# Performance work log

Hardware: AMD Instinct MI355X
Metric: run time of the kernel (lower is better)

## Reference

```python
import jax, jax.numpy as jnp
import numpy as np

B, T, D, H, S = 512, 256, 128, 128, 32


def _param(key, shape, scale):
    return (jax.random.normal(key, shape, dtype=jnp.float32) * scale)


def setup_inputs() -> dict:
    key = jax.random.key(0)
    ks = jax.random.split(key, 32)
    sD = 1.0 / np.sqrt(D)
    sH = 1.0 / np.sqrt(H)
    inp = {
        'x': jax.random.normal(ks[0], (B, T, D), dtype=jnp.float32),
        'statics': jax.random.normal(ks[1], (B, S), dtype=jnp.float32),
        'mask': (jax.random.uniform(ks[2], (B, T, D)) > 0.5).astype(jnp.float32),
        'delta': jax.random.uniform(ks[3], (B, T, D), dtype=jnp.float32),
        'x_last_observed': jax.random.normal(ks[4], (B, T, D), dtype=jnp.float32),
        'x_mean': jax.random.normal(ks[5], (B, D), dtype=jnp.float32),
        'hs0': jax.random.normal(ks[6], (B, H), dtype=jnp.float32),
        # GRU-D decay params
        'w_dg_x': _param(ks[7], (D,), sD), 'b_dg_x': jnp.zeros((D,), jnp.float32),
        'W_dg_h': _param(ks[8], (H, D), sD), 'b_dg_h': jnp.zeros((H,), jnp.float32),
        # gates: update z, reset r, candidate h
        'W_z': _param(ks[9], (H, D), sD), 'U_z': _param(ks[10], (H, H), sH),
        'V_z': _param(ks[11], (H, D), sD), 'b_z': jnp.zeros((H,), jnp.float32),
        'W_r': _param(ks[12], (H, D), sD), 'U_r': _param(ks[13], (H, H), sH),
        'V_r': _param(ks[14], (H, D), sD), 'b_r': jnp.zeros((H,), jnp.float32),
        'W_h': _param(ks[15], (H, D), sD), 'U_h': _param(ks[16], (H, H), sH),
        'V_h': _param(ks[17], (H, D), sD), 'b_h': jnp.zeros((H,), jnp.float32),
        # classifier
        'W_out': _param(ks[18], (1, H + S), 1.0 / np.sqrt(H + S)),
        'b_out': jnp.zeros((1,), jnp.float32),
    }
    return inp


def reference(x, statics, mask, delta, x_last_observed, x_mean, hs0,
              w_dg_x, b_dg_x, W_dg_h, b_dg_h,
              W_z, U_z, V_z, b_z, W_r, U_r, V_r, b_r,
              W_h, U_h, V_h, b_h, W_out, b_out):
    # scan over time: inputs [T, B, D]
    xs = jnp.transpose(x, (1, 0, 2))
    ms = jnp.transpose(mask, (1, 0, 2))
    ds = jnp.transpose(delta, (1, 0, 2))
    xl = jnp.transpose(x_last_observed, (1, 0, 2))

    def step(h, inputs):
        xv, m, d, xlast = inputs
        gamma_x = jnp.exp(-jax.nn.relu(w_dg_x * d + b_dg_x))            # [B, D]
        gamma_h = jnp.exp(-jax.nn.relu(d @ W_dg_h.T + b_dg_h))          # [B, H]
        x_hat = m * xv + (1.0 - m) * (gamma_x * xlast + (1.0 - gamma_x) * x_mean)
        h = gamma_h * h
        z = jax.nn.sigmoid(x_hat @ W_z.T + h @ U_z.T + m @ V_z.T + b_z)
        r = jax.nn.sigmoid(x_hat @ W_r.T + h @ U_r.T + m @ V_r.T + b_r)
        h_tilde = jnp.tanh(x_hat @ W_h.T + (r * h) @ U_h.T + m @ V_h.T + b_h)
        h = (1.0 - z) * h + z * h_tilde
        return h, None

    h_final, _ = jax.lax.scan(step, hs0, (xs, ms, ds, xl))
    full = jnp.concatenate([h_final, statics], axis=1)                  # [B, H+S]
    predictions = full @ W_out.T + b_out                                # [B, 1]
    return predictions
```

## Files before the change

### kernel.cpp

```cpp
#include <hip/hip_runtime.h>
#include <stdint.h>


#define B_ 512
#define T_ 256
#define D_ 128
#define H_ 128
#define S_ 32
#define NE 512
#define KA 384
#define M_ (B_*T_)
#define HP 136
#define ESLAB ((size_t)NE * 16)
#define ESTRIDE ((size_t)32 * ESLAB)

typedef __attribute__((ext_vector_type(8))) short short8;
typedef __attribute__((ext_vector_type(4))) float f32x4;

#define BAR_LDS() asm volatile("s_waitcnt lgkmcnt(0)\n\ts_barrier" ::: "memory")

__device__ __forceinline__ unsigned short f2bf(float f) {
  union { float f; uint32_t u; } v; v.f = f;
  return (unsigned short)((v.u + 0x7FFFu + ((v.u >> 16) & 1u)) >> 16);
}
__device__ __forceinline__ unsigned short f2bf_fast(float f) {
  union { float f; uint32_t u; } v; v.f = f;
  return (unsigned short)((v.u + 0x8000u) >> 16);
}
__device__ __forceinline__ float bf2f(uint32_t s) {
  union { uint32_t u; float f; } v; v.u = s << 16;
  return v.f;
}

__device__ __forceinline__ uint2  ldraw(const unsigned short* p) { return *(const uint2*)p; }
__device__ __forceinline__ float4 ldraw(const float* p)          { return *(const float4*)p; }
__device__ __forceinline__ void unp(uint2 v, float o[4]) {
  o[0] = bf2f(v.x & 0xffffu); o[1] = bf2f(v.x >> 16);
  o[2] = bf2f(v.y & 0xffffu); o[3] = bf2f(v.y >> 16);
}
__device__ __forceinline__ void unp(float4 v, float o[4]) {
  o[0] = v.x; o[1] = v.y; o[2] = v.z; o[3] = v.w;
}
__device__ __forceinline__ void st4(unsigned short* p, const float v[4]) {
  uint2 u;
  u.x = (uint32_t)f2bf(v[0]) | ((uint32_t)f2bf(v[1]) << 16);
  u.y = (uint32_t)f2bf(v[2]) | ((uint32_t)f2bf(v[3]) << 16);
  *(uint2*)p = u;
}
__device__ __forceinline__ void st4(float* p, const float v[4]) {
  *(float4*)p = make_float4(v[0], v[1], v[2], v[3]);
}

__device__ __forceinline__ float fsigmoid(float x) {
  return __builtin_amdgcn_rcpf(1.f + __expf(-x));
}
__device__ __forceinline__ float ftanh(float x) {
  return 1.f - 2.f * __builtin_amdgcn_rcpf(1.f + __expf(2.f * x));
}

#define ASYNC_CP16(gsrc, ldst) \
  __builtin_amdgcn_global_load_lds((const __attribute__((address_space(1))) void*)(gsrc), \
                                   (__attribute__((address_space(3))) void*)(ldst), 16, 0, 0)

__global__ void prep_weights(const float* __restrict__ Wz, const float* __restrict__ Vz,
                             const float* __restrict__ Wr, const float* __restrict__ Vr,
                             const float* __restrict__ Wh, const float* __restrict__ Vh,
                             const float* __restrict__ Wdgh,
                             const float* __restrict__ bz, const float* __restrict__ br,
                             const float* __restrict__ bh, const float* __restrict__ bdgh,
                             unsigned short* __restrict__ Wcat, float* __restrict__ bias)
{
  int id = blockIdx.x * 256 + threadIdx.x;
  if (id < NE * KA) {
    int n = id / KA, k = id - n * KA;
    float v = 0.f;
    if (n < 384) {
      int nn = n & 127;
      const float* W = (n < 128) ? Wz : (n < 256) ? Wr : Wh;
      const float* V = (n < 128) ? Vz : (n < 256) ? Vr : Vh;
      if (k < 128)      v = W[nn * 128 + k];
      else if (k < 256) v = V[nn * 128 + (k - 128)];
    } else {
      if (k >= 256) v = Wdgh[(n - 384) * 128 + (k - 256)];
    }
    Wcat[id] = f2bf(v);
  }
  if (id < NE) {
    bias[id] = (id < 128) ? bz[id] : (id < 256) ? br[id - 128]
             : (id < 384) ? bh[id - 256] : bdgh[id - 384];
  }
}

__global__ void build_A(const float* __restrict__ x, const float* __restrict__ mask,
                        const float* __restrict__ delta, const float* __restrict__ xlast,
                        const float* __restrict__ xmean,
                        const float* __restrict__ wdgx, const float* __restrict__ bdgx,
                        unsigned short* __restrict__ Abuf)
{
  int id = blockIdx.x * 256 + threadIdx.x;
  int m = id >> 5;
  int c = id & 31;
  int t = m >> 9;
  int b = m & (B_ - 1);
  int k = c * 4;
  size_t src = ((size_t)b * T_ + t) * D_ + k;
  float4 xv = *(const float4*)(x + src);
  float4 mv = *(const float4*)(mask + src);
  float4 dv = *(const float4*)(delta + src);
  float4 lv = *(const float4*)(xlast + src);
  float4 uv = *(const float4*)(xmean + (size_t)b * D_ + k);
  float4 wv = *(const float4*)(wdgx + k);
  float4 bv = *(const float4*)(bdgx + k);
  const float* xp = (const float*)&xv; const float* mp = (const float*)&mv;
  const float* dp = (const float*)&dv; const float* lp = (const float*)&lv;
  const float* up = (const float*)&uv; const float* wp = (const float*)&wv;
  const float* bp = (const float*)&bv;
  unsigned short xh[4], mm[4], dd[4];
  #pragma unroll
  for (int i = 0; i < 4; ++i) {
    float g = __expf(-fmaxf(wp[i] * dp[i] + bp[i], 0.f));
    float xhat = mp[i] * xp[i] + (1.f - mp[i]) * (g * lp[i] + (1.f - g) * up[i]);
    xh[i] = f2bf(xhat); mm[i] = f2bf(mp[i]); dd[i] = f2bf(dp[i]);
  }
  uint2 px, pm, pd;
  px.x = (uint32_t)xh[0] | ((uint32_t)xh[1] << 16); px.y = (uint32_t)xh[2] | ((uint32_t)xh[3] << 16);
  pm.x = (uint32_t)mm[0] | ((uint32_t)mm[1] << 16); pm.y = (uint32_t)mm[2] | ((uint32_t)mm[3] << 16);
  pd.x = (uint32_t)dd[0] | ((uint32_t)dd[1] << 16); pd.y = (uint32_t)dd[2] | ((uint32_t)dd[3] << 16);
  unsigned short* rowp = Abuf + (size_t)m * KA;
  *(uint2*)(rowp + k)       = px;
  *(uint2*)(rowp + 128 + k) = pm;
  *(uint2*)(rowp + 256 + k) = pd;
}

template <typename ET>
__global__ __launch_bounds__(256, 2) void gemm_phase1(
    const unsigned short* __restrict__ Abuf, const unsigned short* __restrict__ Wcat,
    const float* __restrict__ bias, ET* __restrict__ E)
{
  __shared__ unsigned short As[3][4096];
  __shared__ unsigned short Bs[3][4096];
  const int tid = threadIdx.x;
  const int wave = tid >> 6, lane = tid & 63;
  const int q = lane >> 4, rl = lane & 15;
  const int m0 = blockIdx.x * 128;
  const int n0 = blockIdx.y * 128;
  const int wm = (wave >> 1) * 64, wn = (wave & 1) * 64;

  f32x4 acc[4][4];
  #pragma unroll
  for (int a = 0; a < 4; ++a)
    #pragma unroll
    for (int b = 0; b < 4; ++b) acc[a][b] = (f32x4){0.f, 0.f, 0.f, 0.f};

  #define STAGE(kt_) do {                                                     \
    const int kbase_ = (kt_) * 32; const int buf_ = (kt_) % 3;                \
    _Pragma("unroll")                                                         \
    for (int i = 0; i < 2; ++i) {                                             \
      int chunk = i * 256 + wave * 64 + lane;                                 \
      int row = chunk >> 2, kc = chunk & 3;                                   \
      ASYNC_CP16(Abuf + (size_t)(m0 + row) * KA + kbase_ + kc * 8,            \
                 &As[buf_][(i * 256 + wave * 64) * 8]);                       \
      ASYNC_CP16(Wcat + (size_t)(n0 + row) * KA + kbase_ + kc * 8,            \
                 &Bs[buf_][(i * 256 + wave * 64) * 8]);                       \
    }                                                                         \
  } while (0)

  STAGE(0);
  STAGE(1);

  #pragma unroll
  for (int kt = 0; kt < 12; ++kt) {
    if (kt == 11) asm volatile("s_waitcnt vmcnt(0)" ::: "memory");
    else          asm volatile("s_waitcnt vmcnt(4)" ::: "memory");
    asm volatile("s_barrier" ::: "memory");
    if (kt < 10) STAGE(kt + 2);
    const int buf = kt % 3;
    short8 af[4], bfr[4];
    #pragma unroll
    for (int tm = 0; tm < 4; ++tm)
      af[tm] = *(const short8*)(&As[buf][(wm + tm * 16 + rl) * 32 + q * 8]);
    #pragma unroll
    for (int tn = 0; tn < 4; ++tn)
      bfr[tn] = *(const short8*)(&Bs[buf][(wn + tn * 16 + rl) * 32 + q * 8]);
    #pragma unroll
    for (int tm = 0; tm < 4; ++tm)
      #pragma unroll
      for (int tn = 0; tn < 4; ++tn)
        acc[tm][tn] = __builtin_amdgcn_mfma_f32_16x16x32_bf16(af[tm], bfr[tn], acc[tm][tn], 0, 0, 0);
  }
  #undef STAGE

  const int t = m0 >> 9;
  const int bbase = m0 & (B_ - 1);
  #pragma unroll
  for (int tn = 0; tn < 4; ++tn) {
    int n = n0 + wn + tn * 16 + rl;
    float bv = bias[n];
    bool isg = (n >= 384);
    #pragma unroll
    for (int tm = 0; tm < 4; ++tm) {
      int brow = bbase + wm + tm * 16;
      float v[4];
      #pragma unroll
      for (int reg = 0; reg < 4; ++reg) {
        float xv = acc[tm][tn][reg] + bv;
        v[reg] = isg ? __expf(-fmaxf(xv, 0.f)) : xv;
      }
      st4(E + ((size_t)t * 32 + (brow >> 4)) * ESLAB + (size_t)n * 16 + q * 4, v);
    }
  }
}

template <typename ET>
__global__ __launch_bounds__(512, 2) void grud_scan(
    const ET* __restrict__ E,
    const float* __restrict__ Uz, const float* __restrict__ Ur, const float* __restrict__ Uh,
    const float* __restrict__ hs0, const float* __restrict__ statics,
    const float* __restrict__ Wout, const float* __restrict__ bout,
    float* __restrict__ out)
{
  __shared__ unsigned short hdec[16 * HP];
  __shared__ unsigned short rhb[16 * HP];
  __shared__ float hfin[16 * HP];
  const int tid = threadIdx.x;
  const int wave = tid >> 6, lane = tid & 63;
  const int q = lane >> 4, rl = lane & 15;
  const int col = wave * 16 + rl;
  const int b0 = blockIdx.x * 16;

  short8 uz[4], ur[4], uh[4];
  #pragma unroll
  for (int kc = 0; kc < 4; ++kc) {
    int koff = kc * 32 + q * 8;
    const float* pzw = Uz + col * H_ + koff;
    const float* prw = Ur + col * H_ + koff;
    const float* phw = Uh + col * H_ + koff;
    #pragma unroll
    for (int j = 0; j < 8; ++j) {
      uz[kc][j] = (short)f2bf(pzw[j]);
      ur[kc][j] = (short)f2bf(prw[j]);
      uh[kc][j] = (short)f2bf(phw[j]);
    }
  }

  const ET* pz = E + (size_t)blockIdx.x * ESLAB + (size_t)col * 16 + q * 4;
  const ET* pr = pz + 128 * 16;
  const ET* ph = pz + 256 * 16;
  const ET* pg = pz + 384 * 16;

  using RawT = decltype(ldraw((const ET*)nullptr));
  RawT cz, cr, chh, cg, nz{}, nr{}, nh{}, ng{};
  cz  = ldraw(pz);
  cr  = ldraw(pr);
  chh = ldraw(ph);
  cg  = ldraw(pg + ESTRIDE);
  RawT g0raw = ldraw(pg);

  float hd[4], g0[4];
  unp(g0raw, g0);
  #pragma unroll
  for (int reg = 0; reg < 4; ++reg) {
    int row = q * 4 + reg;
    float h0 = hs0[(b0 + row) * H_ + col];
    hd[reg] = g0[reg] * h0;
    hdec[row * HP + col] = f2bf_fast(hd[reg]);
  }
  BAR_LDS();

  for (int t = 0; t < T_; ++t) {
    if (t + 1 < T_) {
      size_t off = (size_t)(t + 1) * ESTRIDE;
      nz = ldraw(pz + off); nr = ldraw(pr + off); nh = ldraw(ph + off);
      if (t + 2 < T_) ng = ldraw(pg + (size_t)(t + 2) * ESTRIDE);
    }
    float Pz[4], Pr[4], Ph[4];
    unp(cz, Pz); unp(cr, Pr); unp(chh, Ph);

    short8 af[4];
    #pragma unroll
    for (int kc = 0; kc < 4; ++kc)
      af[kc] = *(const short8*)(&hdec[rl * HP + kc * 32 + q * 8]);
    f32x4 accz = (f32x4){0.f,0.f,0.f,0.f}, accr = (f32x4){0.f,0.f,0.f,0.f};
    #pragma unroll
    for (int kc = 0; kc < 4; ++kc) {
      accz = __builtin_amdgcn_mfma_f32_16x16x32_bf16(af[kc], uz[kc], accz, 0, 0, 0);
      accr = __builtin_amdgcn_mfma_f32_16x16x32_bf16(af[kc], ur[kc], accr, 0, 0, 0);
    }
    float zz[4];
    #pragma unroll
    for (int reg = 0; reg < 4; ++reg) {
      zz[reg] = fsigmoid(accz[reg] + Pz[reg]);
      float rr = fsigmoid(accr[reg] + Pr[reg]);
      rhb[(q * 4 + reg) * HP + col] = f2bf_fast(rr * hd[reg]);
    }
    BAR_LDS();

    short8 ar[4];
    #pragma unroll
    for (int kc = 0; kc < 4; ++kc)
      ar[kc] = *(const short8*)(&rhb[rl * HP + kc * 32 + q * 8]);
    f32x4 acch = (f32x4){0.f,0.f,0.f,0.f};
    #pragma unroll
    for (int kc = 0; kc < 4; ++kc)
      acch = __builtin_amdgcn_mfma_f32_16x16x32_bf16(ar[kc], uh[kc], acch, 0, 0, 0);

    if (t < T_ - 1) {
      float Gn[4];
      unp(cg, Gn);
      #pragma unroll
      for (int reg = 0; reg < 4; ++reg) {
        float ht = ftanh(acch[reg] + Ph[reg]);
        float hn = hd[reg] + zz[reg] * (ht - hd[reg]);
        hd[reg] = Gn[reg] * hn;
        hdec[(q * 4 + reg) * HP + col] = f2bf_fast(hd[reg]);
      }
    } else {
      #pragma unroll
      for (int reg = 0; reg < 4; ++reg) {
        float ht = ftanh(acch[reg] + Ph[reg]);
        float hn = hd[reg] + zz[reg] * (ht - hd[reg]);
        hfin[(q * 4 + reg) * HP + col] = hn;
      }
    }
    BAR_LDS();

    cz = nz; cr = nr; chh = nh; cg = ng;
  }

  {
    int row = tid >> 5, j = tid & 31;
    float acc = 0.f;
    #pragma unroll
    for (int c0 = 0; c0 < 4; ++c0)
      acc += hfin[row * HP + j + c0 * 32] * Wout[j + c0 * 32];
    acc += statics[(size_t)(b0 + row) * S_ + j] * Wout[H_ + j];
    #pragma unroll
    for (int off = 16; off >= 1; off >>= 1)
      acc += __shfl_down(acc, off, 32);
    if (j == 0) out[b0 + row] = acc + bout[0];
  }
}

template <typename ET>
static void launch_all(void* const* d_in, float* out, char* ws, hipStream_t stream)
{
  const float* x      = (const float*)d_in[0];
  const float* statics= (const float*)d_in[1];
  const float* mask   = (const float*)d_in[2];
  const float* delta  = (const float*)d_in[3];
  const float* xlast  = (const float*)d_in[4];
  const float* xmean  = (const float*)d_in[5];
  const float* hs0    = (const float*)d_in[6];
  const float* wdgx   = (const float*)d_in[7];
  const float* bdgx   = (const float*)d_in[8];
  const float* Wdgh   = (const float*)d_in[9];
  const float* bdgh   = (const float*)d_in[10];
  const float* Wz     = (const float*)d_in[11];
  const float* Uz     = (const float*)d_in[12];
  const float* Vz     = (const float*)d_in[13];
  const float* bz     = (const float*)d_in[14];
  const float* Wr     = (const float*)d_in[15];
  const float* Ur     = (const float*)d_in[16];
  const float* Vr     = (const float*)d_in[17];
  const float* br     = (const float*)d_in[18];
  const float* Wh     = (const float*)d_in[19];
  const float* Uh     = (const float*)d_in[20];
  const float* Vh     = (const float*)d_in[21];
  const float* bh     = (const float*)d_in[22];
  const float* Wout   = (const float*)d_in[23];
  const float* bout   = (const float*)d_in[24];

  const size_t eBytes = (size_t)M_ * NE * sizeof(ET);
  const size_t aBytes = (size_t)M_ * KA * 2;
  const size_t wBytes = (size_t)NE * KA * 2;
  ET* E = (ET*)ws;
  unsigned short* Abuf = (unsigned short*)(ws + eBytes);
  unsigned short* Wcat = (unsigned short*)(ws + eBytes + aBytes);
  float* bias = (float*)(ws + eBytes + aBytes + wBytes);

  prep_weights<<<768, 256, 0, stream>>>(Wz, Vz, Wr, Vr, Wh, Vh, Wdgh,
                                        bz, br, bh, bdgh, Wcat, bias);
  build_A<<<(M_ * 32) / 256, 256, 0, stream>>>(x, mask, delta, xlast, xmean,
                                               wdgx, bdgx, Abuf);
  gemm_phase1<ET><<<dim3(M_ / 128, NE / 128), 256, 0, stream>>>(Abuf, Wcat, bias, E);
  grud_scan<ET><<<B_ / 16, 512, 0, stream>>>(E, Uz, Ur, Uh, hs0, statics, Wout, bout, out);
}

extern "C" void kernel_launch(void* const* d_in, const int* in_sizes, int n_in,
                              void* d_out, int out_size, void* d_ws, size_t ws_size,
                              hipStream_t stream)
{
  char* ws = (char*)d_ws;
  float* out = (float*)d_out;
  const size_t common = (size_t)M_ * KA * 2 + (size_t)NE * KA * 2 + 8192;
  const size_t needF32 = (size_t)M_ * NE * 4 + common;
  const size_t needBF  = (size_t)M_ * NE * 2 + common;
  if (ws_size >= needF32)     launch_all<float>(d_in, out, ws, stream);
  else if (ws_size >= needBF) launch_all<unsigned short>(d_in, out, ws, stream);
}
```

Measured before the change: 597.5 us.

## Skip zero K-tiles for decay-gate GEMM block and halve scan waves

In the input-projection GEMM, the column block that computes the hidden-state decay gate now starts at K-tile 8. Those output columns depend only on the delta section of the concatenated input, so the x-hat and mask tiles are never loaded or multiplied there. The loop is no longer fully unrolled, which makes the triple-buffer index dynamic, and the occupancy hint is raised. The recurrent scan kernel drops from 8 waves to 4 per block, with each wave handling two 16-column groups, to make the three block barriers per timestep cheaper. It also moves the z-gate sigmoid after the first barrier so it can overlap the h-candidate MFMAs, at the cost of more registers per thread.

```diff
diff --git a/kernel.cpp b/kernel.cpp
--- a/kernel.cpp
+++ b/kernel.cpp
@@ -133,7 +133,7 @@
 }
 
 template <typename ET>
-__global__ __launch_bounds__(256, 2) void gemm_phase1(
+__global__ __launch_bounds__(256, 3) void gemm_phase1(
     const unsigned short* __restrict__ Abuf, const unsigned short* __restrict__ Wcat,
     const float* __restrict__ bias, ET* __restrict__ E)
 {
@@ -145,6 +145,7 @@
   const int m0 = blockIdx.x * 128;
   const int n0 = blockIdx.y * 128;
   const int wm = (wave >> 1) * 64, wn = (wave & 1) * 64;
+  const int kt0 = (blockIdx.y == 3) ? 8 : 0;
 
   f32x4 acc[4][4];
   #pragma unroll
@@ -165,11 +166,10 @@
     }                                                                         \
   } while (0)
 
-  STAGE(0);
-  STAGE(1);
-
-  #pragma unroll
-  for (int kt = 0; kt < 12; ++kt) {
+  STAGE(kt0);
+  STAGE(kt0 + 1);
+
+  for (int kt = kt0; kt < 12; ++kt) {
     if (kt == 11) asm volatile("s_waitcnt vmcnt(0)" ::: "memory");
     else          asm volatile("s_waitcnt vmcnt(4)" ::: "memory");
     asm volatile("s_barrier" ::: "memory");
@@ -212,7 +212,7 @@
 }
 
 template <typename ET>
-__global__ __launch_bounds__(512, 2) void grud_scan(
+__global__ __launch_bounds__(256, 1) void grud_scan(
     const ET* __restrict__ E,
     const float* __restrict__ Uz, const float* __restrict__ Ur, const float* __restrict__ Uh,
     const float* __restrict__ hs0, const float* __restrict__ statics,
@@ -225,73 +225,91 @@
   const int tid = threadIdx.x;
   const int wave = tid >> 6, lane = tid & 63;
   const int q = lane >> 4, rl = lane & 15;
-  const int col = wave * 16 + rl;
+  const int col0 = wave * 32 + rl;
   const int b0 = blockIdx.x * 16;
 
-  short8 uz[4], ur[4], uh[4];
-  #pragma unroll
-  for (int kc = 0; kc < 4; ++kc) {
-    int koff = kc * 32 + q * 8;
-    const float* pzw = Uz + col * H_ + koff;
-    const float* prw = Ur + col * H_ + koff;
-    const float* phw = Uh + col * H_ + koff;
-    #pragma unroll
-    for (int j = 0; j < 8; ++j) {
-      uz[kc][j] = (short)f2bf(pzw[j]);
-      ur[kc][j] = (short)f2bf(prw[j]);
-      uh[kc][j] = (short)f2bf(phw[j]);
-    }
-  }
-
-  const ET* pz = E + (size_t)blockIdx.x * ESLAB + (size_t)col * 16 + q * 4;
-  const ET* pr = pz + 128 * 16;
-  const ET* ph = pz + 256 * 16;
-  const ET* pg = pz + 384 * 16;
+  short8 uz[2][4], ur[2][4], uh[2][4];
+  #pragma unroll
+  for (int g = 0; g < 2; ++g) {
+    int ncol = col0 + g * 16;
+    #pragma unroll
+    for (int kc = 0; kc < 4; ++kc) {
+      int koff = kc * 32 + q * 8;
+      const float* pzw = Uz + ncol * H_ + koff;
+      const float* prw = Ur + ncol * H_ + koff;
+      const float* phw = Uh + ncol * H_ + koff;
+      #pragma unroll
+      for (int j = 0; j < 8; ++j) {
+        uz[g][kc][j] = (short)f2bf(pzw[j]);
+        ur[g][kc][j] = (short)f2bf(prw[j]);
+        uh[g][kc][j] = (short)f2bf(phw[j]);
+      }
+    }
+  }
+
+  const ET* pz[2]; const ET* pr[2]; const ET* ph[2]; const ET* pg[2];
+  #pragma unroll
+  for (int g = 0; g < 2; ++g) {
+    const ET* base = E + (size_t)blockIdx.x * ESLAB + (size_t)(col0 + g * 16) * 16 + q * 4;
+    pz[g] = base; pr[g] = base + 128 * 16; ph[g] = base + 256 * 16; pg[g] = base + 384 * 16;
+  }
 
   using RawT = decltype(ldraw((const ET*)nullptr));
-  RawT cz, cr, chh, cg, nz{}, nr{}, nh{}, ng{};
-  cz  = ldraw(pz);
-  cr  = ldraw(pr);
-  chh = ldraw(ph);
-  cg  = ldraw(pg + ESTRIDE);
-  RawT g0raw = ldraw(pg);
-
-  float hd[4], g0[4];
-  unp(g0raw, g0);
-  #pragma unroll
-  for (int reg = 0; reg < 4; ++reg) {
-    int row = q * 4 + reg;
-    float h0 = hs0[(b0 + row) * H_ + col];
-    hd[reg] = g0[reg] * h0;
-    hdec[row * HP + col] = f2bf_fast(hd[reg]);
+  RawT cz[2], cr[2], chh[2], cg[2], nz[2], nr[2], nh[2], ng[2];
+  float hd[2][4];
+  #pragma unroll
+  for (int g = 0; g < 2; ++g) {
+    cz[g]  = ldraw(pz[g]);
+    cr[g]  = ldraw(pr[g]);
+    chh[g] = ldraw(ph[g]);
+    cg[g]  = ldraw(pg[g] + ESTRIDE);
+    RawT g0raw = ldraw(pg[g]);
+    float g0[4];
+    unp(g0raw, g0);
+    #pragma unroll
+    for (int reg = 0; reg < 4; ++reg) {
+      int row = q * 4 + reg;
+      float h0 = hs0[(b0 + row) * H_ + col0 + g * 16];
+      hd[g][reg] = g0[reg] * h0;
+      hdec[row * HP + col0 + g * 16] = f2bf_fast(hd[g][reg]);
+    }
   }
   BAR_LDS();
 
   for (int t = 0; t < T_; ++t) {
     if (t + 1 < T_) {
       size_t off = (size_t)(t + 1) * ESTRIDE;
-      nz = ldraw(pz + off); nr = ldraw(pr + off); nh = ldraw(ph + off);
-      if (t + 2 < T_) ng = ldraw(pg + (size_t)(t + 2) * ESTRIDE);
-    }
-    float Pz[4], Pr[4], Ph[4];
-    unp(cz, Pz); unp(cr, Pr); unp(chh, Ph);
+      #pragma unroll
+      for (int g = 0; g < 2; ++g) {
+        nz[g] = ldraw(pz[g] + off); nr[g] = ldraw(pr[g] + off); nh[g] = ldraw(ph[g] + off);
+        if (t + 2 < T_) ng[g] = ldraw(pg[g] + (size_t)(t + 2) * ESTRIDE);
+      }
+    }
 
     short8 af[4];
     #pragma unroll
     for (int kc = 0; kc < 4; ++kc)
       af[kc] = *(const short8*)(&hdec[rl * HP + kc * 32 + q * 8]);
-    f32x4 accz = (f32x4){0.f,0.f,0.f,0.f}, accr = (f32x4){0.f,0.f,0.f,0.f};
+    f32x4 accz[2], accr[2];
+    #pragma unroll
+    for (int g = 0; g < 2; ++g) { accz[g] = (f32x4){0,0,0,0}; accr[g] = (f32x4){0,0,0,0}; }
     #pragma unroll
     for (int kc = 0; kc < 4; ++kc) {
-      accz = __builtin_amdgcn_mfma_f32_16x16x32_bf16(af[kc], uz[kc], accz, 0, 0, 0);
-      accr = __builtin_amdgcn_mfma_f32_16x16x32_bf16(af[kc], ur[kc], accr, 0, 0, 0);
-    }
-    float zz[4];
-    #pragma unroll
-    for (int reg = 0; reg < 4; ++reg) {
-      zz[reg] = fsigmoid(accz[reg] + Pz[reg]);
-      float rr = fsigmoid(accr[reg] + Pr[reg]);
-      rhb[(q * 4 + reg) * HP + col] = f2bf_fast(rr * hd[reg]);
+      #pragma unroll
+      for (int g = 0; g < 2; ++g) {
+        accz[g] = __builtin_amdgcn_mfma_f32_16x16x32_bf16(af[kc], uz[g][kc], accz[g], 0, 0, 0);
+        accr[g] = __builtin_amdgcn_mfma_f32_16x16x32_bf16(af[kc], ur[g][kc], accr[g], 0, 0, 0);
+      }
+    }
+    #pragma unroll
+    for (int g = 0; g < 2; ++g) {
+      float Pr[4];
+      unp(cr[g], Pr);
+      #pragma unroll
+      for (int reg = 0; reg < 4; ++reg) {
+        float rr = fsigmoid(accr[g][reg] + Pr[reg]);
+        rhb[(q * 4 + reg) * HP + col0 + g * 16] = f2bf_fast(rr * hd[g][reg]);
+      }
     }
     BAR_LDS();
 
@@ -299,44 +317,68 @@
     #pragma unroll
     for (int kc = 0; kc < 4; ++kc)
       ar[kc] = *(const short8*)(&rhb[rl * HP + kc * 32 + q * 8]);
-    f32x4 acch = (f32x4){0.f,0.f,0.f,0.f};
+    float zz[2][4];
+    #pragma unroll
+    for (int g = 0; g < 2; ++g) {
+      float Pz[4];
+      unp(cz[g], Pz);
+      #pragma unroll
+      for (int reg = 0; reg < 4; ++reg)
+        zz[g][reg] = fsigmoid(accz[g][reg] + Pz[reg]);
+    }
+    f32x4 acch[2];
+    #pragma unroll
+    for (int g = 0; g < 2; ++g) acch[g] = (f32x4){0,0,0,0};
     #pragma unroll
     for (int kc = 0; kc < 4; ++kc)
-      acch = __builtin_amdgcn_mfma_f32_16x16x32_bf16(ar[kc], uh[kc], acch, 0, 0, 0);
+      #pragma unroll
+      for (int g = 0; g < 2; ++g)
+        acch[g] = __builtin_amdgcn_mfma_f32_16x16x32_bf16(ar[kc], uh[g][kc], acch[g], 0, 0, 0);
 
     if (t < T_ - 1) {
-      float Gn[4];
-      unp(cg, Gn);
-      #pragma unroll
-      for (int reg = 0; reg < 4; ++reg) {
-        float ht = ftanh(acch[reg] + Ph[reg]);
-        float hn = hd[reg] + zz[reg] * (ht - hd[reg]);
-        hd[reg] = Gn[reg] * hn;
-        hdec[(q * 4 + reg) * HP + col] = f2bf_fast(hd[reg]);
+      #pragma unroll
+      for (int g = 0; g < 2; ++g) {
+        float Ph[4], Gn[4];
+        unp(chh[g], Ph); unp(cg[g], Gn);
+        #pragma unroll
+        for (int reg = 0; reg < 4; ++reg) {
+          float ht = ftanh(acch[g][reg] + Ph[reg]);
+          float hn = hd[g][reg] + zz[g][reg] * (ht - hd[g][reg]);
+          hd[g][reg] = Gn[reg] * hn;
+          hdec[(q * 4 + reg) * HP + col0 + g * 16] = f2bf_fast(hd[g][reg]);
+        }
       }
     } else {
       #pragma unroll
-      for (int reg = 0; reg < 4; ++reg) {
-        float ht = ftanh(acch[reg] + Ph[reg]);
-        float hn = hd[reg] + zz[reg] * (ht - hd[reg]);
-        hfin[(q * 4 + reg) * HP + col] = hn;
+      for (int g = 0; g < 2; ++g) {
+        float Ph[4];
+        unp(chh[g], Ph);
+        #pragma unroll
+        for (int reg = 0; reg < 4; ++reg) {
+          float ht = ftanh(acch[g][reg] + Ph[reg]);
+          float hn = hd[g][reg] + zz[g][reg] * (ht - hd[g][reg]);
+          hfin[(q * 4 + reg) * HP + col0 + g * 16] = hn;
+        }
       }
     }
     BAR_LDS();
 
-    cz = nz; cr = nr; chh = nh; cg = ng;
+    #pragma unroll
+    for (int g = 0; g < 2; ++g) { cz[g] = nz[g]; cr[g] = nr[g]; chh[g] = nh[g]; cg[g] = ng[g]; }
   }
 
   {
-    int row = tid >> 5, j = tid & 31;
+    int row = tid >> 4, j = tid & 15;
     float acc = 0.f;
     #pragma unroll
-    for (int c0 = 0; c0 < 4; ++c0)
-      acc += hfin[row * HP + j + c0 * 32] * Wout[j + c0 * 32];
-    acc += statics[(size_t)(b0 + row) * S_ + j] * Wout[H_ + j];
-    #pragma unroll
-    for (int off = 16; off >= 1; off >>= 1)
-      acc += __shfl_down(acc, off, 32);
+    for (int c0 = 0; c0 < 8; ++c0)
+      acc += hfin[row * HP + j + c0 * 16] * Wout[j + c0 * 16];
+    #pragma unroll
+    for (int c0 = 0; c0 < 2; ++c0)
+      acc += statics[(size_t)(b0 + row) * S_ + j + c0 * 16] * Wout[H_ + j + c0 * 16];
+    #pragma unroll
+    for (int off = 8; off >= 1; off >>= 1)
+      acc += __shfl_down(acc, off, 16);
     if (j == 0) out[b0 + row] = acc + bout[0];
   }
 }
@@ -383,7 +425,7 @@
   build_A<<<(M_ * 32) / 256, 256, 0, stream>>>(x, mask, delta, xlast, xmean,
                                                wdgx, bdgx, Abuf);
   gemm_phase1<ET><<<dim3(M_ / 128, NE / 128), 256, 0, stream>>>(Abuf, Wcat, bias, E);
-  grud_scan<ET><<<B_ / 16, 512, 0, stream>>>(E, Uz, Ur, Uh, hs0, statics, Wout, bout, out);
+  grud_scan<ET><<<B_ / 16, 256, 0, stream>>>(E, Uz, Ur, Uh, hs0, statics, Wout, bout, out);
 }
 
 extern "C" void kernel_launch(void* const* d_in, const int* in_sizes, int n_in,
```

Result: slower. 661.7 us (+10.8%).
